# Optimization experiments

Hardware: AMD Instinct MI355X
Metric: run time of the kernel (lower is better)

## Reference

```python
import jax, jax.numpy as jnp
import numpy as np

B, T = 8192, 26
V, E, H, L = 23, 100, 128, 64  # vocab, emb dim, GRU hidden, latent; LSTM hidden = E


def setup_inputs() -> dict:
    key = jax.random.key(0)
    ks = jax.random.split(key, 16)
    rn = lambda k, shape, scale=0.1: (jax.random.normal(k, shape, jnp.float32) * scale)
    emb = rn(ks[0], (V, E)).at[0].set(0.0)  # padding_idx=0 row zeroed
    return {
        "z": jax.random.normal(ks[1], (B, L), jnp.float32),
        "x_in": jax.random.randint(ks[2], (B, T), 0, V),
        "emb": emb,
        "fc_z_w": rn(ks[3], (H, L)), "fc_z_b": rn(ks[4], (H,)),
        "gru_wih": rn(ks[5], (3 * H, E)), "gru_whh": rn(ks[6], (3 * H, H)),
        "gru_bih": rn(ks[7], (3 * H,)), "gru_bhh": rn(ks[8], (3 * H,)),
        "lstm_wih": rn(ks[9], (4 * E, H)), "lstm_whh": rn(ks[10], (4 * E, E)),
        "lstm_bih": rn(ks[11], (4 * E,)), "lstm_bhh": rn(ks[12], (4 * E,)),
        "out_w": rn(ks[13], (V, E)), "out_b": rn(ks[14], (V,)),
    }


def _gru(e, h0, Wih, Whh, bih, bhh):
    # e: (B,T,E); precompute input projections for all steps, scan over T.
    xg = jnp.einsum('bti,gi->btg', e, Wih) + bih  # (B,T,3H)

    def step(h, x):
        hg = h @ Whh.T + bhh
        xr, xz, xn = jnp.split(x, 3, axis=-1)
        hr, hz, hn = jnp.split(hg, 3, axis=-1)
        r = jax.nn.sigmoid(xr + hr)
        zg = jax.nn.sigmoid(xz + hz)
        n = jnp.tanh(xn + r * hn)
        h_new = (1.0 - zg) * n + zg * h
        return h_new, h_new

    _, ys = jax.lax.scan(step, h0, jnp.swapaxes(xg, 0, 1))  # (T,B,H)
    return jnp.swapaxes(ys, 0, 1)


def _lstm(x, h0, c0, Wih, Whh, bih, bhh):
    xg = jnp.einsum('bti,gi->btg', x, Wih) + bih  # (B,T,4E)

    def step(hc, xt):
        h, c = hc
        g = xt + h @ Whh.T + bhh
        i, f, gg, o = jnp.split(g, 4, axis=-1)
        c_new = jax.nn.sigmoid(f) * c + jax.nn.sigmoid(i) * jnp.tanh(gg)
        h_new = jax.nn.sigmoid(o) * jnp.tanh(c_new)
        return (h_new, c_new), h_new

    _, ys = jax.lax.scan(step, (h0, c0), jnp.swapaxes(xg, 0, 1))
    return jnp.swapaxes(ys, 0, 1)


def reference(z, x_in, emb, fc_z_w, fc_z_b, gru_wih, gru_whh, gru_bih, gru_bhh,
              lstm_wih, lstm_whh, lstm_bih, lstm_bhh, out_w, out_b):
    h0 = jnp.tanh(z @ fc_z_w.T + fc_z_b)            # (B,H)
    e = emb[x_in]                                    # (B,T,E)
    y = _gru(e, h0, gru_wih, gru_whh, gru_bih, gru_bhh)           # (B,T,H)
    zeros = jnp.zeros((z.shape[0], E), dtype=z.dtype)
    y = _lstm(y, zeros, zeros, lstm_wih, lstm_whh, lstm_bih, lstm_bhh)  # (B,T,E)
    logits = jnp.einsum('bte,ve->btv', y, out_w) + out_b          # (B,T,V)
    return logits
```

## Files before the change

kernel.cpp:

```cpp
#include <hip/hip_runtime.h>
#include <stdint.h>
#include <stddef.h>

#define BB 8192
#define TT 26
#define VV 23
#define EE 100
#define HH 128
#define LL 64

typedef __attribute__((ext_vector_type(8))) short bf16x8;
typedef __attribute__((ext_vector_type(4))) float f32x4;

#define MFMA(a, b, c) __builtin_amdgcn_mfma_f32_16x16x32_bf16((a), (b), (c), 0, 0, 0)

#define OFF_GRUW   0ull
#define OFF_TBL    98304ull
#define OFF_LSTMW  122880ull
#define OFF_OUTW   352256ull
#define OFF_FCZW   360448ull
#define OFF_LBIAS  376832ull
#define OFF_Y      379904ull

__device__ __forceinline__ void force_frag(bf16x8& v) { asm volatile("" : "+v"(v)); }

__device__ __forceinline__ unsigned short f2bf(float f) {
  union { float f; unsigned u; } v; v.f = f;
  unsigned u = v.u;
  return (unsigned short)((u + 0x7FFFu + ((u >> 16) & 1u)) >> 16);
}
__device__ __forceinline__ unsigned short f2bf_fast(float f) {
  union { float f; unsigned u; } v; v.f = f;
  return (unsigned short)((v.u + 0x8000u) >> 16);
}
#define LOG2E 1.4426950408889634f
__device__ __forceinline__ float sigm(float x) {
  return __builtin_amdgcn_rcpf(1.0f + __builtin_amdgcn_exp2f(-x * LOG2E));
}
__device__ __forceinline__ float tanh_(float x) {
  return __builtin_fmaf(-2.0f,
      __builtin_amdgcn_rcpf(1.0f + __builtin_amdgcn_exp2f(x * (2.0f * LOG2E))), 1.0f);
}

__global__ __launch_bounds__(512) void prep_table_kernel(
    const float* __restrict__ emb, const float* __restrict__ gru_wih,
    const float* __restrict__ gru_bih, char* __restrict__ ws)
{
  __shared__ float emb_s[VV * EE];
  __shared__ float wih_s[16 * EE];
  __shared__ float bih_s[16];
  const int tid = threadIdx.x;
  const int ct  = blockIdx.x;
  const int n0  = ct * 16;

  for (int i = tid; i < VV * EE; i += 512) emb_s[i] = emb[i];
  for (int i = tid; i < 16 * EE; i += 512) wih_s[i] = gru_wih[n0 * EE + i];
  if (tid < 16) bih_s[tid] = gru_bih[n0 + tid];
  __syncthreads();

  const int j    = tid & 7;
  const int lane = (tid >> 3) & 63;
  const int n16  = lane & 15;
  const int k    = ((lane >> 4) & 3) * 8 + j;
  float v = 0.0f;
  if (k < VV) {
    const float* ep = emb_s + k * EE;
    const float* wp = wih_s + n16 * EE;
    float s0 = 0.f, s1 = 0.f, s2 = 0.f, s3 = 0.f;
#pragma unroll 5
    for (int m = 0; m < EE; m += 4) {
      s0 += ep[m] * wp[m];         s1 += ep[m + 1] * wp[m + 1];
      s2 += ep[m + 2] * wp[m + 2]; s3 += ep[m + 3] * wp[m + 3];
    }
    v = bih_s[n16] + ((s0 + s1) + (s2 + s3));
  }
  *(unsigned short*)(ws + OFF_TBL + (size_t)(ct * 512 + tid) * 2) = f2bf(v);
}

__global__ __launch_bounds__(256) void prep_main_kernel(
    const float* __restrict__ fc_z_w, const float* __restrict__ gru_whh,
    const float* __restrict__ lstm_wih, const float* __restrict__ lstm_whh,
    const float* __restrict__ lstm_bih, const float* __restrict__ lstm_bhh,
    const float* __restrict__ out_w, char* __restrict__ ws)
{
  int e = blockIdx.x * 256 + threadIdx.x;

  if (e < 49152) {
    int j = e & 7, lane = (e >> 3) & 63, kc = (e >> 9) & 3, ct = e >> 11;
    int n = ct * 16 + (lane & 15);
    int k = kc * 32 + ((lane >> 4) & 3) * 8 + j;
    *(unsigned short*)(ws + OFF_GRUW + (size_t)e * 2) = f2bf(gru_whh[n * HH + k]);
    return;
  }
  e -= 49152;
  if (e < 114688) {
    int j = e & 7, lane = (e >> 3) & 63, kc = (e >> 9) & 7, ct = e >> 12;
    int row = ct * 16 + (lane & 15);
    int g = row / 112, c = row % 112;
    int q = (lane >> 4) & 3;
    float v = 0.0f;
    if (c < EE) {
      if (kc < 4) {
        int k = kc * 32 + q * 8 + j;
        v = lstm_wih[(g * EE + c) * HH + k];
      } else {
        int k = (kc - 4) * 32 + q * 8 + j;
        if (k < EE) v = lstm_whh[(g * EE + c) * EE + k];
      }
    }
    *(unsigned short*)(ws + OFF_LSTMW + (size_t)e * 2) = f2bf(v);
    return;
  }
  e -= 114688;
  if (e < 4096) {
    int j = e & 7, lane = (e >> 3) & 63, kc = (e >> 9) & 3, ct = e >> 11;
    int n = ct * 16 + (lane & 15);
    int k = kc * 32 + ((lane >> 4) & 3) * 8 + j;
    float v = (n < VV && k < EE) ? out_w[n * EE + k] : 0.0f;
    *(unsigned short*)(ws + OFF_OUTW + (size_t)e * 2) = f2bf(v);
    return;
  }
  e -= 4096;
  if (e < 8192) {
    int j = e & 7, lane = (e >> 3) & 63, kc = (e >> 9) & 1, ct = e >> 10;
    int n = ct * 16 + (lane & 15);
    int k = kc * 32 + ((lane >> 4) & 3) * 8 + j;
    *(unsigned short*)(ws + OFF_FCZW + (size_t)e * 2) = f2bf(fc_z_w[n * LL + k]);
    return;
  }
  e -= 8192;
  if (e < 448) {
    int g = e / 112, c = e % 112;
    float v = (c < EE) ? (lstm_bih[g * EE + c] + lstm_bhh[g * EE + c]) : 0.0f;
    *(float*)(ws + OFF_LBIAS + (size_t)e * 4) = v;
  }
}

__global__ __launch_bounds__(512, 4) void gru_kernel(
    const float* __restrict__ z, const int* __restrict__ x_in,
    const float* __restrict__ fc_z_b, const float* __restrict__ gru_bhh,
    const unsigned short* __restrict__ gruw, const unsigned short* __restrict__ tbl,
    const unsigned short* __restrict__ fczw, unsigned short* __restrict__ yout)
{
  __shared__ unsigned short hfrag[2][2048];
  __shared__ unsigned char idx_lds[TT * 16];
  const int tid  = threadIdx.x;
  const int wv   = tid >> 6;
  const int lane = tid & 63;
  const int l15  = lane & 15;
  const int q    = (lane >> 4) & 3;
  const int blk  = blockIdx.x;

  for (int i = tid; i < TT * 16; i += 512) {
    int t = i >> 4, r = i & 15;
    idx_lds[i] = (unsigned char)x_in[(blk * 16 + r) * TT + t];
  }

  bf16x8 gw[3][4], tw[3];
#pragma unroll
  for (int g = 0; g < 3; g++) {
    int ct = g * 8 + wv;
#pragma unroll
    for (int kc = 0; kc < 4; kc++) {
      gw[g][kc] = *(const bf16x8*)(gruw + (size_t)(ct * 4 + kc) * 512 + lane * 8);
      force_frag(gw[g][kc]);
    }
    tw[g] = *(const bf16x8*)(tbl + (size_t)ct * 512 + lane * 8);
    force_frag(tw[g]);
  }
  const int col = wv * 16 + l15;
  const float b_r = gru_bhh[0 * HH + col];
  const float b_z = gru_bhh[1 * HH + col];
  const float b_n = gru_bhh[2 * HH + col];
  const int wbase = (col >> 5) * 512 + ((col >> 3) & 3) * 128 + (col & 7);

  float h[4];
  {
    bf16x8 fw0 = *(const bf16x8*)(fczw + (size_t)(wv * 2 + 0) * 512 + lane * 8);
    bf16x8 fw1 = *(const bf16x8*)(fczw + (size_t)(wv * 2 + 1) * 512 + lane * 8);
    const float* zp = z + (size_t)(blk * 16 + l15) * LL + q * 8;
    f32x4 z0 = *(const f32x4*)(zp);
    f32x4 z1 = *(const f32x4*)(zp + 4);
    f32x4 z2 = *(const f32x4*)(zp + 32);
    f32x4 z3 = *(const f32x4*)(zp + 36);
    bf16x8 za0, za1;
#pragma unroll
    for (int j = 0; j < 4; j++) {
      za0[j]     = (short)f2bf(z0[j]);
      za0[4 + j] = (short)f2bf(z1[j]);
      za1[j]     = (short)f2bf(z2[j]);
      za1[4 + j] = (short)f2bf(z3[j]);
    }
    float fzb = fc_z_b[col];
    f32x4 acc = {fzb, fzb, fzb, fzb};
    acc = MFMA(za0, fw0, acc);
    acc = MFMA(za1, fw1, acc);
#pragma unroll
    for (int i = 0; i < 4; i++) {
      h[i] = tanh_(acc[i]);
      hfrag[0][wbase + (q * 4 + i) * 8] = f2bf_fast(h[i]);
    }
  }
  __syncthreads();

  int cur = 0;
  for (int t = 0; t < TT; t++) {
    if (t > 0 && wv < 4) {
      bf16x8 yv = *(const bf16x8*)((const char*)hfrag[cur] + wv * 1024 + lane * 16);
      *(bf16x8*)(yout + ((size_t)(blk * TT + (t - 1)) * 4 + wv) * 512 + lane * 8) = yv;
    }
    int iv = idx_lds[t * 16 + l15];
    bf16x8 oh;
#pragma unroll
    for (int j = 0; j < 8; j++)
      oh[j] = (short)((iv == q * 8 + j) ? 0x3F80 : 0);

    f32x4 ar  = {b_r, b_r, b_r, b_r};
    f32x4 az  = {b_z, b_z, b_z, b_z};
    f32x4 ahn = {b_n, b_n, b_n, b_n};
    f32x4 axn = {0.0f, 0.0f, 0.0f, 0.0f};
    ar  = MFMA(oh, tw[0], ar);
    az  = MFMA(oh, tw[1], az);
    axn = MFMA(oh, tw[2], axn);

    bf16x8 a[4];
#pragma unroll
    for (int kc = 0; kc < 4; kc++)
      a[kc] = *(const bf16x8*)((const char*)hfrag[cur] + kc * 1024 + lane * 16);
#pragma unroll
    for (int kc = 0; kc < 4; kc++) {
      ar  = MFMA(a[kc], gw[0][kc], ar);
      az  = MFMA(a[kc], gw[1][kc], az);
      ahn = MFMA(a[kc], gw[2][kc], ahn);
    }

    int nb = cur ^ 1;
#pragma unroll
    for (int i = 0; i < 4; i++) {
      float r  = sigm(ar[i]);
      float zg = sigm(az[i]);
      float n  = tanh_(__builtin_fmaf(r, ahn[i], axn[i]));
      h[i] = __builtin_fmaf(zg, h[i] - n, n);
      hfrag[nb][wbase + (q * 4 + i) * 8] = f2bf_fast(h[i]);
    }
    __syncthreads();
    cur = nb;
  }
  if (wv < 4) {
    bf16x8 yv = *(const bf16x8*)((const char*)hfrag[cur] + wv * 1024 + lane * 16);
    *(bf16x8*)(yout + ((size_t)(blk * TT + (TT - 1)) * 4 + wv) * 512 + lane * 8) = yv;
  }
}

__global__ __launch_bounds__(512, 2) void lstm_kernel(
    const unsigned short* __restrict__ lstmw, const float* __restrict__ lbias,
    const unsigned short* __restrict__ ybuf,
    const float* __restrict__ out_b, const unsigned short* __restrict__ outw,
    float* __restrict__ out)
{
  __shared__ unsigned short hbuf[2][2][2048];
  const int tid  = threadIdx.x;
  const int wv   = tid >> 6;
  const int lane = tid & 63;
  const int l15  = lane & 15;
  const int q    = (lane >> 4) & 3;
  const int blk  = blockIdx.x;

  for (int i = tid; i < 2 * 2 * 2048; i += 512)
    ((unsigned short*)hbuf)[i] = 0;

  if (wv < 7) {
    bf16x8 lw[4][8];
#pragma unroll
    for (int g = 0; g < 4; g++)
#pragma unroll
      for (int kc = 0; kc < 8; kc++) {
        lw[g][kc] = *(const bf16x8*)(lstmw + (size_t)((g * 7 + wv) * 8 + kc) * 512 + lane * 8);
        force_frag(lw[g][kc]);
      }
    const int col = wv * 16 + l15;
    float b[4];
#pragma unroll
    for (int g = 0; g < 4; g++) b[g] = lbias[g * 112 + col];
    const int wbase = (col >> 5) * 512 + ((col >> 3) & 3) * 128 + (col & 7);
    float c[2][4] = {{0, 0, 0, 0}, {0, 0, 0, 0}};
    __syncthreads();

    f32x4 yacc[2][4];
#pragma unroll
    for (int s = 0; s < 2; s++) {
      bf16x8 ya[4];
#pragma unroll
      for (int kc = 0; kc < 4; kc++)
        ya[kc] = *(const bf16x8*)(ybuf + ((size_t)((blk * 2 + s) * TT + 0) * 4 + kc) * 512 + lane * 8);
#pragma unroll
      for (int g = 0; g < 4; g++) yacc[s][g] = (f32x4){b[g], b[g], b[g], b[g]};
#pragma unroll
      for (int kc = 0; kc < 4; kc++) {
        yacc[s][0] = MFMA(ya[kc], lw[0][kc], yacc[s][0]);
        yacc[s][1] = MFMA(ya[kc], lw[1][kc], yacc[s][1]);
        yacc[s][2] = MFMA(ya[kc], lw[2][kc], yacc[s][2]);
        yacc[s][3] = MFMA(ya[kc], lw[3][kc], yacc[s][3]);
      }
    }

    for (int p = 0; p < TT; p++) {
      const int pn = (p + 1 < TT) ? (p + 1) : (TT - 1);
#pragma unroll
      for (int s = 0; s < 2; s++) {
        bf16x8 ha[4];
#pragma unroll
        for (int kc = 0; kc < 4; kc++)
          ha[kc] = *(const bf16x8*)&hbuf[p & 1][s][kc * 512 + lane * 8];
#pragma unroll
        for (int kc = 0; kc < 4; kc++) {
          yacc[s][0] = MFMA(ha[kc], lw[0][kc + 4], yacc[s][0]);
          yacc[s][1] = MFMA(ha[kc], lw[1][kc + 4], yacc[s][1]);
          yacc[s][2] = MFMA(ha[kc], lw[2][kc + 4], yacc[s][2]);
          yacc[s][3] = MFMA(ha[kc], lw[3][kc + 4], yacc[s][3]);
        }
      }
      bf16x8 yan[2][4];
#pragma unroll
      for (int s = 0; s < 2; s++)
#pragma unroll
        for (int kc = 0; kc < 4; kc++)
          yan[s][kc] = *(const bf16x8*)(ybuf + ((size_t)((blk * 2 + s) * TT + pn) * 4 + kc) * 512 + lane * 8);
#pragma unroll
      for (int s = 0; s < 2; s++) {
#pragma unroll
        for (int i = 0; i < 4; i++) {
          float ii = sigm(yacc[s][0][i]), ff = sigm(yacc[s][1][i]);
          float gg = tanh_(yacc[s][2][i]), oo = sigm(yacc[s][3][i]);
          float cn = __builtin_fmaf(ff, c[s][i], ii * gg);
          c[s][i] = cn;
          hbuf[(p + 1) & 1][s][wbase + (q * 4 + i) * 8] = f2bf_fast(oo * tanh_(cn));
        }
      }
#pragma unroll
      for (int s = 0; s < 2; s++) {
#pragma unroll
        for (int g = 0; g < 4; g++) yacc[s][g] = (f32x4){b[g], b[g], b[g], b[g]};
#pragma unroll
        for (int kc = 0; kc < 4; kc++) {
          yacc[s][0] = MFMA(yan[s][kc], lw[0][kc], yacc[s][0]);
          yacc[s][1] = MFMA(yan[s][kc], lw[1][kc], yacc[s][1]);
          yacc[s][2] = MFMA(yan[s][kc], lw[2][kc], yacc[s][2]);
          yacc[s][3] = MFMA(yan[s][kc], lw[3][kc], yacc[s][3]);
        }
      }
      __syncthreads();
    }
    __syncthreads();
  } else {
    bf16x8 ow[2][4];
#pragma unroll
    for (int ct = 0; ct < 2; ct++)
#pragma unroll
      for (int kc = 0; kc < 4; kc++) {
        ow[ct][kc] = *(const bf16x8*)(outw + (size_t)(ct * 4 + kc) * 512 + lane * 8);
        force_frag(ow[ct][kc]);
      }
    float ob[2];
#pragma unroll
    for (int ct = 0; ct < 2; ct++) {
      int cv = ct * 16 + l15;
      ob[ct] = (cv < VV) ? out_b[cv] : 0.0f;
    }
    __syncthreads();

    for (int p = 0; p <= TT; p++) {
      if (p >= 1) {
        const int t = p - 1;
#pragma unroll
        for (int s = 0; s < 2; s++) {
          bf16x8 ha[4];
#pragma unroll
          for (int kc = 0; kc < 4; kc++)
            ha[kc] = *(const bf16x8*)&hbuf[p & 1][s][kc * 512 + lane * 8];
#pragma unroll
          for (int ct = 0; ct < 2; ct++) {
            f32x4 acc = {ob[ct], ob[ct], ob[ct], ob[ct]};
#pragma unroll
            for (int kc = 0; kc < 4; kc++)
              acc = MFMA(ha[kc], ow[ct][kc], acc);
            int cv = ct * 16 + l15;
            if (cv < VV) {
#pragma unroll
              for (int i = 0; i < 4; i++) {
                int rowg = blk * 32 + s * 16 + q * 4 + i;
                out[((size_t)rowg * TT + t) * VV + cv] = acc[i];
              }
            }
          }
        }
      }
      __syncthreads();
    }
  }
}

extern "C" void kernel_launch(void* const* d_in, const int* in_sizes, int n_in,
                              void* d_out, int out_size, void* d_ws, size_t ws_size,
                              hipStream_t stream) {
  (void)in_sizes; (void)n_in; (void)out_size; (void)ws_size;
  const float* z        = (const float*)d_in[0];
  const int*   x_in     = (const int*)  d_in[1];
  const float* emb      = (const float*)d_in[2];
  const float* fc_z_w   = (const float*)d_in[3];
  const float* fc_z_b   = (const float*)d_in[4];
  const float* gru_wih  = (const float*)d_in[5];
  const float* gru_whh  = (const float*)d_in[6];
  const float* gru_bih  = (const float*)d_in[7];
  const float* gru_bhh  = (const float*)d_in[8];
  const float* lstm_wih = (const float*)d_in[9];
  const float* lstm_whh = (const float*)d_in[10];
  const float* lstm_bih = (const float*)d_in[11];
  const float* lstm_bhh = (const float*)d_in[12];
  const float* out_w    = (const float*)d_in[13];
  const float* out_b    = (const float*)d_in[14];
  char*  ws  = (char*)d_ws;
  float* out = (float*)d_out;

  const unsigned short* gruw  = (const unsigned short*)(ws + OFF_GRUW);
  const unsigned short* tblp  = (const unsigned short*)(ws + OFF_TBL);
  const unsigned short* lstmw = (const unsigned short*)(ws + OFF_LSTMW);
  const unsigned short* outw  = (const unsigned short*)(ws + OFF_OUTW);
  const unsigned short* fczw  = (const unsigned short*)(ws + OFF_FCZW);
  const float*          lbias = (const float*)(ws + OFF_LBIAS);
  unsigned short*       ybuf  = (unsigned short*)(ws + OFF_Y);

  prep_main_kernel<<<690, 256, 0, stream>>>(fc_z_w, gru_whh, lstm_wih, lstm_whh,
                                            lstm_bih, lstm_bhh, out_w, ws);
  prep_table_kernel<<<24, 512, 0, stream>>>(emb, gru_wih, gru_bih, ws);
  gru_kernel<<<512, 512, 0, stream>>>(z, x_in, fc_z_b, gru_bhh,
                                      gruw, tblp, fczw, ybuf);
  lstm_kernel<<<256, 512, 0, stream>>>(lstmw, lbias, ybuf, out_b, outw, out);
}
```

Before: 190.1 us.

## Fuse GRU, LSTM and output projection into one wavefront-pipelined kernel

Merges the GRU and LSTM kernels into one 1024-thread block. Eight waves run the GRU, seven run the LSTM, and one runs the output projection, pipelined one timestep apart through LDS double buffers. This removes the global round trip of the bf16 GRU output and one kernel launch. In exchange the LSTM now handles 16 rows per block instead of 32, each step waits on a block-wide barrier across all three stages, and 1024-thread blocks with large register-resident weights may limit occupancy.

```diff
diff --git a/kernel.cpp b/kernel.cpp
--- a/kernel.cpp
+++ b/kernel.cpp
@@ -20,7 +20,6 @@
 #define OFF_OUTW   352256ull
 #define OFF_FCZW   360448ull
 #define OFF_LBIAS  376832ull
-#define OFF_Y      379904ull
 
 __device__ __forceinline__ void force_frag(bf16x8& v) { asm volatile("" : "+v"(v)); }
 
@@ -136,13 +135,17 @@
   }
 }
 
-__global__ __launch_bounds__(512, 4) void gru_kernel(
+__global__ __launch_bounds__(1024, 4) void fused_kernel(
     const float* __restrict__ z, const int* __restrict__ x_in,
     const float* __restrict__ fc_z_b, const float* __restrict__ gru_bhh,
     const unsigned short* __restrict__ gruw, const unsigned short* __restrict__ tbl,
-    const unsigned short* __restrict__ fczw, unsigned short* __restrict__ yout)
+    const unsigned short* __restrict__ fczw,
+    const unsigned short* __restrict__ lstmw, const float* __restrict__ lbias,
+    const float* __restrict__ out_b, const unsigned short* __restrict__ outw,
+    float* __restrict__ out)
 {
   __shared__ unsigned short hfrag[2][2048];
+  __shared__ unsigned short lhbuf[2][2048];
   __shared__ unsigned char idx_lds[TT * 16];
   const int tid  = threadIdx.x;
   const int wv   = tid >> 6;
@@ -151,207 +154,156 @@
   const int q    = (lane >> 4) & 3;
   const int blk  = blockIdx.x;
 
-  for (int i = tid; i < TT * 16; i += 512) {
-    int t = i >> 4, r = i & 15;
-    idx_lds[i] = (unsigned char)x_in[(blk * 16 + r) * TT + t];
-  }
-
-  bf16x8 gw[3][4], tw[3];
-#pragma unroll
-  for (int g = 0; g < 3; g++) {
-    int ct = g * 8 + wv;
-#pragma unroll
-    for (int kc = 0; kc < 4; kc++) {
-      gw[g][kc] = *(const bf16x8*)(gruw + (size_t)(ct * 4 + kc) * 512 + lane * 8);
-      force_frag(gw[g][kc]);
-    }
-    tw[g] = *(const bf16x8*)(tbl + (size_t)ct * 512 + lane * 8);
-    force_frag(tw[g]);
-  }
-  const int col = wv * 16 + l15;
-  const float b_r = gru_bhh[0 * HH + col];
-  const float b_z = gru_bhh[1 * HH + col];
-  const float b_n = gru_bhh[2 * HH + col];
-  const int wbase = (col >> 5) * 512 + ((col >> 3) & 3) * 128 + (col & 7);
-
-  float h[4];
-  {
-    bf16x8 fw0 = *(const bf16x8*)(fczw + (size_t)(wv * 2 + 0) * 512 + lane * 8);
-    bf16x8 fw1 = *(const bf16x8*)(fczw + (size_t)(wv * 2 + 1) * 512 + lane * 8);
-    const float* zp = z + (size_t)(blk * 16 + l15) * LL + q * 8;
-    f32x4 z0 = *(const f32x4*)(zp);
-    f32x4 z1 = *(const f32x4*)(zp + 4);
-    f32x4 z2 = *(const f32x4*)(zp + 32);
-    f32x4 z3 = *(const f32x4*)(zp + 36);
-    bf16x8 za0, za1;
-#pragma unroll
-    for (int j = 0; j < 4; j++) {
-      za0[j]     = (short)f2bf(z0[j]);
-      za0[4 + j] = (short)f2bf(z1[j]);
-      za1[j]     = (short)f2bf(z2[j]);
-      za1[4 + j] = (short)f2bf(z3[j]);
-    }
-    float fzb = fc_z_b[col];
-    f32x4 acc = {fzb, fzb, fzb, fzb};
-    acc = MFMA(za0, fw0, acc);
-    acc = MFMA(za1, fw1, acc);
-#pragma unroll
-    for (int i = 0; i < 4; i++) {
-      h[i] = tanh_(acc[i]);
-      hfrag[0][wbase + (q * 4 + i) * 8] = f2bf_fast(h[i]);
-    }
-  }
-  __syncthreads();
-
-  int cur = 0;
-  for (int t = 0; t < TT; t++) {
-    if (t > 0 && wv < 4) {
-      bf16x8 yv = *(const bf16x8*)((const char*)hfrag[cur] + wv * 1024 + lane * 16);
-      *(bf16x8*)(yout + ((size_t)(blk * TT + (t - 1)) * 4 + wv) * 512 + lane * 8) = yv;
-    }
-    int iv = idx_lds[t * 16 + l15];
-    bf16x8 oh;
-#pragma unroll
-    for (int j = 0; j < 8; j++)
-      oh[j] = (short)((iv == q * 8 + j) ? 0x3F80 : 0);
-
-    f32x4 ar  = {b_r, b_r, b_r, b_r};
-    f32x4 az  = {b_z, b_z, b_z, b_z};
-    f32x4 ahn = {b_n, b_n, b_n, b_n};
-    f32x4 axn = {0.0f, 0.0f, 0.0f, 0.0f};
-    ar  = MFMA(oh, tw[0], ar);
-    az  = MFMA(oh, tw[1], az);
-    axn = MFMA(oh, tw[2], axn);
-
-    bf16x8 a[4];
-#pragma unroll
-    for (int kc = 0; kc < 4; kc++)
-      a[kc] = *(const bf16x8*)((const char*)hfrag[cur] + kc * 1024 + lane * 16);
-#pragma unroll
-    for (int kc = 0; kc < 4; kc++) {
-      ar  = MFMA(a[kc], gw[0][kc], ar);
-      az  = MFMA(a[kc], gw[1][kc], az);
-      ahn = MFMA(a[kc], gw[2][kc], ahn);
-    }
-
-    int nb = cur ^ 1;
-#pragma unroll
-    for (int i = 0; i < 4; i++) {
-      float r  = sigm(ar[i]);
-      float zg = sigm(az[i]);
-      float n  = tanh_(__builtin_fmaf(r, ahn[i], axn[i]));
-      h[i] = __builtin_fmaf(zg, h[i] - n, n);
-      hfrag[nb][wbase + (q * 4 + i) * 8] = f2bf_fast(h[i]);
+  for (int i = tid; i < 2 * 2048; i += 1024)
+    ((unsigned short*)lhbuf)[i] = 0;
+
+  if (wv < 8) {
+    {
+      int rid = wv * 64 + lane;
+      for (int i = rid; i < TT * 16; i += 512) {
+        int t = i >> 4, r = i & 15;
+        idx_lds[i] = (unsigned char)x_in[(blk * 16 + r) * TT + t];
+      }
+    }
+    bf16x8 gw[3][4], tw[3];
+#pragma unroll
+    for (int g = 0; g < 3; g++) {
+      int ct = g * 8 + wv;
+#pragma unroll
+      for (int kc = 0; kc < 4; kc++) {
+        gw[g][kc] = *(const bf16x8*)(gruw + (size_t)(ct * 4 + kc) * 512 + lane * 8);
+        force_frag(gw[g][kc]);
+      }
+      tw[g] = *(const bf16x8*)(tbl + (size_t)ct * 512 + lane * 8);
+      force_frag(tw[g]);
+    }
+    const int col = wv * 16 + l15;
+    const float b_r = gru_bhh[0 * HH + col];
+    const float b_z = gru_bhh[1 * HH + col];
+    const float b_n = gru_bhh[2 * HH + col];
+    const int wbase = (col >> 5) * 512 + ((col >> 3) & 3) * 128 + (col & 7);
+
+    float h[4];
+    {
+      bf16x8 fw0 = *(const bf16x8*)(fczw + (size_t)(wv * 2 + 0) * 512 + lane * 8);
+      bf16x8 fw1 = *(const bf16x8*)(fczw + (size_t)(wv * 2 + 1) * 512 + lane * 8);
+      const float* zp = z + (size_t)(blk * 16 + l15) * LL + q * 8;
+      f32x4 z0 = *(const f32x4*)(zp);
+      f32x4 z1 = *(const f32x4*)(zp + 4);
+      f32x4 z2 = *(const f32x4*)(zp + 32);
+      f32x4 z3 = *(const f32x4*)(zp + 36);
+      bf16x8 za0, za1;
+#pragma unroll
+      for (int j = 0; j < 4; j++) {
+        za0[j]     = (short)f2bf(z0[j]);
+        za0[4 + j] = (short)f2bf(z1[j]);
+        za1[j]     = (short)f2bf(z2[j]);
+        za1[4 + j] = (short)f2bf(z3[j]);
+      }
+      float fzb = fc_z_b[col];
+      f32x4 acc = {fzb, fzb, fzb, fzb};
+      acc = MFMA(za0, fw0, acc);
+      acc = MFMA(za1, fw1, acc);
+#pragma unroll
+      for (int i = 0; i < 4; i++) {
+        h[i] = tanh_(acc[i]);
+        hfrag[0][wbase + (q * 4 + i) * 8] = f2bf_fast(h[i]);
+      }
     }
     __syncthreads();
-    cur = nb;
-  }
-  if (wv < 4) {
-    bf16x8 yv = *(const bf16x8*)((const char*)hfrag[cur] + wv * 1024 + lane * 16);
-    *(bf16x8*)(yout + ((size_t)(blk * TT + (TT - 1)) * 4 + wv) * 512 + lane * 8) = yv;
-  }
-}
-
-__global__ __launch_bounds__(512, 2) void lstm_kernel(
-    const unsigned short* __restrict__ lstmw, const float* __restrict__ lbias,
-    const unsigned short* __restrict__ ybuf,
-    const float* __restrict__ out_b, const unsigned short* __restrict__ outw,
-    float* __restrict__ out)
-{
-  __shared__ unsigned short hbuf[2][2][2048];
-  const int tid  = threadIdx.x;
-  const int wv   = tid >> 6;
-  const int lane = tid & 63;
-  const int l15  = lane & 15;
-  const int q    = (lane >> 4) & 3;
-  const int blk  = blockIdx.x;
-
-  for (int i = tid; i < 2 * 2 * 2048; i += 512)
-    ((unsigned short*)hbuf)[i] = 0;
-
-  if (wv < 7) {
+
+    for (int p = 0; p < TT + 2; p++) {
+      if (p < TT) {
+        int iv = idx_lds[p * 16 + l15];
+        bf16x8 oh;
+#pragma unroll
+        for (int j = 0; j < 8; j++)
+          oh[j] = (short)((iv == q * 8 + j) ? 0x3F80 : 0);
+
+        f32x4 ar  = {b_r, b_r, b_r, b_r};
+        f32x4 az  = {b_z, b_z, b_z, b_z};
+        f32x4 ahn = {b_n, b_n, b_n, b_n};
+        f32x4 axn = {0.0f, 0.0f, 0.0f, 0.0f};
+        ar  = MFMA(oh, tw[0], ar);
+        az  = MFMA(oh, tw[1], az);
+        axn = MFMA(oh, tw[2], axn);
+
+        bf16x8 a[4];
+#pragma unroll
+        for (int kc = 0; kc < 4; kc++)
+          a[kc] = *(const bf16x8*)((const char*)hfrag[p & 1] + kc * 1024 + lane * 16);
+#pragma unroll
+        for (int kc = 0; kc < 4; kc++) {
+          ar  = MFMA(a[kc], gw[0][kc], ar);
+          az  = MFMA(a[kc], gw[1][kc], az);
+          ahn = MFMA(a[kc], gw[2][kc], ahn);
+        }
+#pragma unroll
+        for (int i = 0; i < 4; i++) {
+          float r  = sigm(ar[i]);
+          float zg = sigm(az[i]);
+          float n  = tanh_(__builtin_fmaf(r, ahn[i], axn[i]));
+          h[i] = __builtin_fmaf(zg, h[i] - n, n);
+          hfrag[(p + 1) & 1][wbase + (q * 4 + i) * 8] = f2bf_fast(h[i]);
+        }
+      }
+      __syncthreads();
+    }
+  } else if (wv < 15) {
+    const int tile = wv - 8;
     bf16x8 lw[4][8];
 #pragma unroll
     for (int g = 0; g < 4; g++)
 #pragma unroll
       for (int kc = 0; kc < 8; kc++) {
-        lw[g][kc] = *(const bf16x8*)(lstmw + (size_t)((g * 7 + wv) * 8 + kc) * 512 + lane * 8);
+        lw[g][kc] = *(const bf16x8*)(lstmw + (size_t)((g * 7 + tile) * 8 + kc) * 512 + lane * 8);
         force_frag(lw[g][kc]);
       }
-    const int col = wv * 16 + l15;
+    const int col = tile * 16 + l15;
     float b[4];
 #pragma unroll
     for (int g = 0; g < 4; g++) b[g] = lbias[g * 112 + col];
     const int wbase = (col >> 5) * 512 + ((col >> 3) & 3) * 128 + (col & 7);
-    float c[2][4] = {{0, 0, 0, 0}, {0, 0, 0, 0}};
+    float c[4] = {0, 0, 0, 0};
     __syncthreads();
 
-    f32x4 yacc[2][4];
-#pragma unroll
-    for (int s = 0; s < 2; s++) {
-      bf16x8 ya[4];
-#pragma unroll
-      for (int kc = 0; kc < 4; kc++)
-        ya[kc] = *(const bf16x8*)(ybuf + ((size_t)((blk * 2 + s) * TT + 0) * 4 + kc) * 512 + lane * 8);
-#pragma unroll
-      for (int g = 0; g < 4; g++) yacc[s][g] = (f32x4){b[g], b[g], b[g], b[g]};
-#pragma unroll
-      for (int kc = 0; kc < 4; kc++) {
-        yacc[s][0] = MFMA(ya[kc], lw[0][kc], yacc[s][0]);
-        yacc[s][1] = MFMA(ya[kc], lw[1][kc], yacc[s][1]);
-        yacc[s][2] = MFMA(ya[kc], lw[2][kc], yacc[s][2]);
-        yacc[s][3] = MFMA(ya[kc], lw[3][kc], yacc[s][3]);
-      }
-    }
-
-    for (int p = 0; p < TT; p++) {
-      const int pn = (p + 1 < TT) ? (p + 1) : (TT - 1);
-#pragma unroll
-      for (int s = 0; s < 2; s++) {
-        bf16x8 ha[4];
-#pragma unroll
-        for (int kc = 0; kc < 4; kc++)
-          ha[kc] = *(const bf16x8*)&hbuf[p & 1][s][kc * 512 + lane * 8];
+    for (int p = 0; p < TT + 2; p++) {
+      if (p >= 1 && p <= TT) {
+        bf16x8 ya[4], ha[4];
 #pragma unroll
         for (int kc = 0; kc < 4; kc++) {
-          yacc[s][0] = MFMA(ha[kc], lw[0][kc + 4], yacc[s][0]);
-          yacc[s][1] = MFMA(ha[kc], lw[1][kc + 4], yacc[s][1]);
-          yacc[s][2] = MFMA(ha[kc], lw[2][kc + 4], yacc[s][2]);
-          yacc[s][3] = MFMA(ha[kc], lw[3][kc + 4], yacc[s][3]);
-        }
-      }
-      bf16x8 yan[2][4];
-#pragma unroll
-      for (int s = 0; s < 2; s++)
-#pragma unroll
-        for (int kc = 0; kc < 4; kc++)
-          yan[s][kc] = *(const bf16x8*)(ybuf + ((size_t)((blk * 2 + s) * TT + pn) * 4 + kc) * 512 + lane * 8);
-#pragma unroll
-      for (int s = 0; s < 2; s++) {
+          ya[kc] = *(const bf16x8*)((const char*)hfrag[p & 1] + kc * 1024 + lane * 16);
+          ha[kc] = *(const bf16x8*)((const char*)lhbuf[(p - 1) & 1] + kc * 1024 + lane * 16);
+        }
+        f32x4 ai = {b[0], b[0], b[0], b[0]};
+        f32x4 af = {b[1], b[1], b[1], b[1]};
+        f32x4 ag = {b[2], b[2], b[2], b[2]};
+        f32x4 ao = {b[3], b[3], b[3], b[3]};
+#pragma unroll
+        for (int kc = 0; kc < 4; kc++) {
+          ai = MFMA(ya[kc], lw[0][kc], ai);
+          af = MFMA(ya[kc], lw[1][kc], af);
+          ag = MFMA(ya[kc], lw[2][kc], ag);
+          ao = MFMA(ya[kc], lw[3][kc], ao);
+        }
+#pragma unroll
+        for (int kc = 0; kc < 4; kc++) {
+          ai = MFMA(ha[kc], lw[0][kc + 4], ai);
+          af = MFMA(ha[kc], lw[1][kc + 4], af);
+          ag = MFMA(ha[kc], lw[2][kc + 4], ag);
+          ao = MFMA(ha[kc], lw[3][kc + 4], ao);
+        }
 #pragma unroll
         for (int i = 0; i < 4; i++) {
-          float ii = sigm(yacc[s][0][i]), ff = sigm(yacc[s][1][i]);
-          float gg = tanh_(yacc[s][2][i]), oo = sigm(yacc[s][3][i]);
-          float cn = __builtin_fmaf(ff, c[s][i], ii * gg);
-          c[s][i] = cn;
-          hbuf[(p + 1) & 1][s][wbase + (q * 4 + i) * 8] = f2bf_fast(oo * tanh_(cn));
-        }
-      }
-#pragma unroll
-      for (int s = 0; s < 2; s++) {
-#pragma unroll
-        for (int g = 0; g < 4; g++) yacc[s][g] = (f32x4){b[g], b[g], b[g], b[g]};
-#pragma unroll
-        for (int kc = 0; kc < 4; kc++) {
-          yacc[s][0] = MFMA(yan[s][kc], lw[0][kc], yacc[s][0]);
-          yacc[s][1] = MFMA(yan[s][kc], lw[1][kc], yacc[s][1]);
-          yacc[s][2] = MFMA(yan[s][kc], lw[2][kc], yacc[s][2]);
-          yacc[s][3] = MFMA(yan[s][kc], lw[3][kc], yacc[s][3]);
+          float ii = sigm(ai[i]), ff = sigm(af[i]);
+          float gg = tanh_(ag[i]), oo = sigm(ao[i]);
+          float cn = __builtin_fmaf(ff, c[i], ii * gg);
+          c[i] = cn;
+          lhbuf[p & 1][wbase + (q * 4 + i) * 8] = f2bf_fast(oo * tanh_(cn));
         }
       }
       __syncthreads();
     }
-    __syncthreads();
   } else {
     bf16x8 ow[2][4];
 #pragma unroll
@@ -369,28 +321,25 @@
     }
     __syncthreads();
 
-    for (int p = 0; p <= TT; p++) {
-      if (p >= 1) {
-        const int t = p - 1;
-#pragma unroll
-        for (int s = 0; s < 2; s++) {
-          bf16x8 ha[4];
+    for (int p = 0; p < TT + 2; p++) {
+      if (p >= 2) {
+        const int t = p - 2;
+        bf16x8 ha[4];
+#pragma unroll
+        for (int kc = 0; kc < 4; kc++)
+          ha[kc] = *(const bf16x8*)((const char*)lhbuf[(p - 1) & 1] + kc * 1024 + lane * 16);
+#pragma unroll
+        for (int ct = 0; ct < 2; ct++) {
+          f32x4 acc = {ob[ct], ob[ct], ob[ct], ob[ct]};
 #pragma unroll
           for (int kc = 0; kc < 4; kc++)
-            ha[kc] = *(const bf16x8*)&hbuf[p & 1][s][kc * 512 + lane * 8];
-#pragma unroll
-          for (int ct = 0; ct < 2; ct++) {
-            f32x4 acc = {ob[ct], ob[ct], ob[ct], ob[ct]};
-#pragma unroll
-            for (int kc = 0; kc < 4; kc++)
-              acc = MFMA(ha[kc], ow[ct][kc], acc);
-            int cv = ct * 16 + l15;
-            if (cv < VV) {
-#pragma unroll
-              for (int i = 0; i < 4; i++) {
-                int rowg = blk * 32 + s * 16 + q * 4 + i;
-                out[((size_t)rowg * TT + t) * VV + cv] = acc[i];
-              }
+            acc = MFMA(ha[kc], ow[ct][kc], acc);
+          int cv = ct * 16 + l15;
+          if (cv < VV) {
+#pragma unroll
+            for (int i = 0; i < 4; i++) {
+              int rowg = blk * 16 + q * 4 + i;
+              out[((size_t)rowg * TT + t) * VV + cv] = acc[i];
             }
           }
         }
@@ -428,12 +377,11 @@
   const unsigned short* outw  = (const unsigned short*)(ws + OFF_OUTW);
   const unsigned short* fczw  = (const unsigned short*)(ws + OFF_FCZW);
   const float*          lbias = (const float*)(ws + OFF_LBIAS);
-  unsigned short*       ybuf  = (unsigned short*)(ws + OFF_Y);
 
   prep_main_kernel<<<690, 256, 0, stream>>>(fc_z_w, gru_whh, lstm_wih, lstm_whh,
                                             lstm_bih, lstm_bhh, out_w, ws);
   prep_table_kernel<<<24, 512, 0, stream>>>(emb, gru_wih, gru_bih, ws);
-  gru_kernel<<<512, 512, 0, stream>>>(z, x_in, fc_z_b, gru_bhh,
-                                      gruw, tblp, fczw, ybuf);
-  lstm_kernel<<<256, 512, 0, stream>>>(lstmw, lbias, ybuf, out_b, outw, out);
-}
+  fused_kernel<<<512, 1024, 0, stream>>>(z, x_in, fc_z_b, gru_bhh,
+                                         gruw, tblp, fczw, lstmw, lbias,
+                                         out_b, outw, out);
+}
```

After: 312.2 us. 1.64x slower.
